# Optimization experiments

Measured on AMD Instinct MI355X. Metric: run time of the kernel, lower is better.

## Reference

```python
import jax, jax.numpy as jnp
import numpy as np

D_MODEL = 1024
H = 16
D_K = D_MODEL // H


def setup_inputs() -> dict:
    key = jax.random.key(0)
    ks = jax.random.split(key, 8)
    B, S = 2, 2048
    q = jax.random.normal(ks[0], (B, S, D_MODEL), dtype=jnp.float32)
    k = jax.random.normal(ks[1], (B, S, D_MODEL), dtype=jnp.float32)
    v = jax.random.normal(ks[2], (B, S, D_MODEL), dtype=jnp.float32)
    mask = jnp.ones((B, 1, S), dtype=jnp.int32)  # key-padding mask, 1 = keep
    sc = 1.0 / np.sqrt(D_MODEL)
    # torch Linear weights [out, in]
    Wq = jax.random.normal(ks[3], (D_MODEL, D_MODEL), dtype=jnp.float32) * sc
    Wk = jax.random.normal(ks[4], (D_MODEL, D_MODEL), dtype=jnp.float32) * sc
    Wv = jax.random.normal(ks[5], (D_MODEL, D_MODEL), dtype=jnp.float32) * sc
    Wo = jax.random.normal(ks[6], (D_MODEL, D_MODEL), dtype=jnp.float32) * sc
    return {"q": q, "k": k, "v": v, "mask": mask,
            "Wq": Wq, "Wk": Wk, "Wv": Wv, "Wo": Wo}


def reference(q, k, v, mask, Wq, Wk, Wv, Wo):
    B, Sq, _ = q.shape
    Sk = k.shape[1]
    # projections (torch Linear: x @ W.T), split heads -> [B, H, S, d_k]
    def split_heads(x, W, S):
        return (x @ W.T).reshape(B, S, H, D_K).transpose(0, 2, 1, 3)
    qh = split_heads(q, Wq, Sq)
    kh = split_heads(k, Wk, Sk)
    vh = split_heads(v, Wv, Sk)
    scores = jnp.einsum('bhqd,bhkd->bhqk', qh, kh) / jnp.sqrt(
        jnp.asarray(D_K, qh.dtype))
    # mask.unsqueeze(1): [B,1,S] -> [B,1,1,S]; masked_fill(mask==0, -1e9)
    m = mask[:, None, :, :]
    scores = jnp.where(m == 0, jnp.asarray(-1e9, scores.dtype), scores)
    p = jax.nn.softmax(scores, axis=-1)
    out = jnp.einsum('bhqk,bhkd->bhqd', p, vh)
    out = out.transpose(0, 2, 1, 3).reshape(B, Sq, H * D_K)
    return out @ Wo.T
```

## Files before the change

### kernel.cpp

```cpp
#include <hip/hip_runtime.h>
#include <hip/hip_bf16.h>

#define LOG2E 1.4426950408889634f

typedef __attribute__((ext_vector_type(8))) __bf16 bf16x8;
typedef __attribute__((ext_vector_type(2))) __bf16 bf16x2;
typedef __attribute__((ext_vector_type(4))) float f32x4;
typedef __attribute__((ext_vector_type(16))) float f32x16;

#define MFMA16(a,b,c) __builtin_amdgcn_mfma_f32_16x16x32_bf16((a),(b),(c),0,0,0)
#define MFMA32(a,b,c) __builtin_amdgcn_mfma_f32_32x32x16_bf16((a),(b),(c),0,0,0)

#define GLL16(g, l) __builtin_amdgcn_global_load_lds( \
    (const __attribute__((address_space(1))) void*)(g), \
    (__attribute__((address_space(3))) void*)(l), 16, 0, 0)

__device__ __forceinline__ unsigned short bfu(float f) {
    __bf16 h = (__bf16)f; unsigned short u; __builtin_memcpy(&u, &h, 2); return u;
}
__device__ __forceinline__ unsigned cvtpk(float lo, float hi) {
    bf16x2 t; t.x = (__bf16)lo; t.y = (__bf16)hi;
    unsigned r; __builtin_memcpy(&r, &t, 4); return r;
}
__device__ __forceinline__ bf16x8 pack4(unsigned a, unsigned b, unsigned c, unsigned d) {
    union { unsigned u[4]; bf16x8 v; } t; t.u[0]=a; t.u[1]=b; t.u[2]=c; t.u[3]=d; return t.v;
}
__device__ __forceinline__ bf16x8 cvt8(float4 a, float4 b, float s) {
    bf16x8 o;
    o[0]=(__bf16)(a.x*s); o[1]=(__bf16)(a.y*s); o[2]=(__bf16)(a.z*s); o[3]=(__bf16)(a.w*s);
    o[4]=(__bf16)(b.x*s); o[5]=(__bf16)(b.y*s); o[6]=(__bf16)(b.z*s); o[7]=(__bf16)(b.w*s);
    return o;
}

__device__ __forceinline__ size_t kidx(int bh, int s, int d) {
    int kt = s>>6, half=(s>>5)&1, l31k=s&31;
    int dc=d>>4, hik=(d>>3)&1, e=d&7;
    return (((size_t)bh*32+kt)*8 + half*4+dc)*512 + (hik*32+l31k)*8 + e;
}
__device__ __forceinline__ size_t vidx(int bh, int s, int d) {
    int kt=s>>6, kvin=s&63, kc=kvin>>4, rem=kvin&15;
    int hiv=(rem>>2)&1, e=(rem&3)+4*(rem>>3);
    int v1=d>>5, l31v=d&31;
    return (((size_t)bh*32+kt)*8 + kc*2+v1)*512 + (hiv*32+l31v)*8 + e;
}

__global__ __launch_bounds__(256)
void conv_kernel(const float* __restrict__ q, const float* __restrict__ k,
                 const float* __restrict__ v, const float* __restrict__ Wq,
                 const float* __restrict__ Wk, const float* __restrict__ Wv,
                 const float* __restrict__ Wo, unsigned short* __restrict__ Xb,
                 unsigned short* __restrict__ Wb)
{
    const int y = blockIdx.y;
    if (y < 3) {
        const float* s = (y==0)?q:(y==1)?k:v;
        size_t i = ((size_t)blockIdx.x*256 + threadIdx.x)*8;
        float4 a = *(const float4*)(s+i), b = *(const float4*)(s+i+4);
        *(bf16x8*)(Xb + (size_t)y*4194304 + i) = cvt8(a, b, 1.0f);
    } else {
        const int w = blockIdx.x >> 9;
        const float* s = (w==0)?Wq:(w==1)?Wk:(w==2)?Wv:Wo;
        const float sc = (w==0) ? 0.125f*LOG2E : 1.0f;
        size_t i = ((size_t)(blockIdx.x & 511)*256 + threadIdx.x)*8;
        float4 a = *(const float4*)(s+i), b = *(const float4*)(s+i+4);
        *(bf16x8*)(Wb + (size_t)w*1048576 + i) = cvt8(a, b, sc);
    }
}

__global__ __launch_bounds__(256)
void qkv_kernel(const unsigned short* __restrict__ Xb,
                const unsigned short* __restrict__ Wb,
                unsigned short* __restrict__ Qh, unsigned short* __restrict__ Kg,
                unsigned short* __restrict__ Vg)
{
    __shared__ unsigned short As[2][4096];
    __shared__ unsigned short Bs[2][4096];
    const int z = blockIdx.z;
    const unsigned short* X = Xb + (size_t)z*4194304;
    const unsigned short* W = Wb + (size_t)z*1048576;
    const int t = threadIdx.x, wid = t>>6, lane = t&63;
    const int m0 = blockIdx.x*128, n0 = blockIdx.y*128;
    const int wr = (wid>>1)*64, wc = (wid&1)*64;
    const int lr = lane&15, lk = lane>>4;

    f32x4 acc[4][4] = {};

#pragma unroll
    for (int i=0;i<2;++i){
        int flat = i*4096 + wid*1024 + lane*16;
        int row = flat>>6, cb = (flat&63) ^ ((row&3)<<4);
        GLL16(X + (size_t)(m0+row)*1024 + (cb>>1), (char*)&As[0][0] + i*4096 + wid*1024);
        GLL16(W + (size_t)(n0+row)*1024 + (cb>>1), (char*)&Bs[0][0] + i*4096 + wid*1024);
    }
    asm volatile("s_waitcnt vmcnt(0)" ::: "memory");
    __builtin_amdgcn_s_barrier();
    asm volatile("" ::: "memory");

    for (int kt=0; kt<32; ++kt){
        const int cur = kt&1;
        if (kt<31){
            const int nb = cur^1, K0 = (kt+1)*32;
#pragma unroll
            for (int i=0;i<2;++i){
                int flat = i*4096 + wid*1024 + lane*16;
                int row = flat>>6, cb = (flat&63) ^ ((row&3)<<4);
                GLL16(X + (size_t)(m0+row)*1024 + K0 + (cb>>1), (char*)&As[nb][0] + i*4096 + wid*1024);
                GLL16(W + (size_t)(n0+row)*1024 + K0 + (cb>>1), (char*)&Bs[nb][0] + i*4096 + wid*1024);
            }
        }
        bf16x8 a[4], b[4];
#pragma unroll
        for (int i=0;i<4;++i){
            int row = wr+i*16+lr;
            a[i] = *(const bf16x8*)((const char*)&As[cur][0] + row*64 + ((lk*16)^((row&3)<<4)));
        }
#pragma unroll
        for (int j=0;j<4;++j){
            int row = wc+j*16+lr;
            b[j] = *(const bf16x8*)((const char*)&Bs[cur][0] + row*64 + ((lk*16)^((row&3)<<4)));
        }
#pragma unroll
        for (int i=0;i<4;++i)
#pragma unroll
            for (int j=0;j<4;++j)
                acc[i][j] = MFMA16(a[i], b[j], acc[i][j]);
        asm volatile("s_waitcnt vmcnt(0)" ::: "memory");
        __builtin_amdgcn_s_barrier();
        asm volatile("" ::: "memory");
    }

#pragma unroll
    for (int i=0;i<4;++i)
#pragma unroll
      for (int j=0;j<4;++j)
#pragma unroll
        for (int r=0;r<4;++r){
            int m = m0 + wr + i*16 + lk*4 + r;
            int n = n0 + wc + j*16 + lr;
            int b_ = m>>11, s = m&2047;
            int h = n>>6, d = n&63;
            int bh = b_*16 + h;
            unsigned short val = bfu(acc[i][j][r]);
            if (z==0)      Qh[((size_t)bh*2048 + s)*64 + d] = val;
            else if (z==1) Kg[kidx(bh, s, d)] = val;
            else           Vg[vidx(bh, s, d)] = val;
        }
}

__global__ __launch_bounds__(256)
void oproj_kernel(const unsigned short* __restrict__ Oh,
                  const unsigned short* __restrict__ Wo,
                  float* __restrict__ out)
{
    __shared__ unsigned short As[2][8192];
    __shared__ unsigned short Bs2[2][4096];
    const int t = threadIdx.x, wid = t>>6, lane = t&63;
    const int m0 = blockIdx.x*128, n0 = blockIdx.y*64;
    const int wr = (wid>>1)*64, wc = (wid&1)*32;
    const int lr = lane&15, lk = lane>>4;
    const int fbase = wid*1024 + lane*16;

    f32x4 acc[4][2] = {};

#pragma unroll
    for (int i=0;i<4;++i){
        int flat = i*4096 + fbase, row = flat>>7;
        int cb = (flat&127) ^ ((row&7)<<4);
        int m = m0+row, b_ = m>>11, s = m&2047;
        GLL16(Oh + ((size_t)(b_*16+0)*2048 + s)*64 + (cb>>1), (char*)&As[0][0] + i*4096 + wid*1024);
    }
#pragma unroll
    for (int i=0;i<2;++i){
        int flat = i*4096 + fbase, row = flat>>7;
        int cb = (flat&127) ^ ((row&7)<<4);
        GLL16(Wo + (size_t)(n0+row)*1024 + (cb>>1), (char*)&Bs2[0][0] + i*4096 + wid*1024);
    }

    for (int kt=0; kt<16; ++kt){
        const int cur = kt&1;
        if (kt<15){
            const int nb = cur^1, K0 = (kt+1)*64, h = K0>>6;
#pragma unroll
            for (int i=0;i<4;++i){
                int flat = i*4096 + fbase, row = flat>>7;
                int cb = (flat&127) ^ ((row&7)<<4);
                int m = m0+row, b_ = m>>11, s = m&2047;
                GLL16(Oh + ((size_t)(b_*16+h)*2048 + s)*64 + (cb>>1),
                      (char*)&As[nb][0] + i*4096 + wid*1024);
            }
#pragma unroll
            for (int i=0;i<2;++i){
                int flat = i*4096 + fbase, row = flat>>7;
                int cb = (flat&127) ^ ((row&7)<<4);
                GLL16(Wo + (size_t)(n0+row)*1024 + K0 + (cb>>1),
                      (char*)&Bs2[nb][0] + i*4096 + wid*1024);
            }
            asm volatile("s_waitcnt vmcnt(6)" ::: "memory");
        } else {
            asm volatile("s_waitcnt vmcnt(0)" ::: "memory");
        }
        __builtin_amdgcn_s_barrier();
        asm volatile("" ::: "memory");

        bf16x8 a[4][2], b[2][2];
#pragma unroll
        for (int i=0;i<4;++i){
            int row = wr+i*16+lr, sw = (row&7)<<4;
            const char* rp = (const char*)&As[cur][0] + row*128;
#pragma unroll
            for (int ks=0;ks<2;++ks)
                a[i][ks] = *(const bf16x8*)(rp + ((ks*64 + lk*16)^sw));
        }
#pragma unroll
        for (int j=0;j<2;++j){
            int row = wc+j*16+lr, sw = (row&7)<<4;
            const char* rp = (const char*)&Bs2[cur][0] + row*128;
#pragma unroll
            for (int ks=0;ks<2;++ks)
                b[j][ks] = *(const bf16x8*)(rp + ((ks*64 + lk*16)^sw));
        }
#pragma unroll
        for (int i=0;i<4;++i)
#pragma unroll
          for (int j=0;j<2;++j)
#pragma unroll
            for (int ks=0;ks<2;++ks)
                acc[i][j] = MFMA16(a[i][ks], b[j][ks], acc[i][j]);
        asm volatile("" ::: "memory");
        __builtin_amdgcn_s_barrier();
    }

#pragma unroll
    for (int i=0;i<4;++i)
#pragma unroll
      for (int j=0;j<2;++j)
#pragma unroll
        for (int r=0;r<4;++r){
            int m = m0 + wr + i*16 + lk*4 + r;
            int n = n0 + wc + j*16 + lr;
            out[(size_t)m*1024 + n] = acc[i][j][r];
        }
}

__global__ __launch_bounds__(256, 2)
void attn_kernel(const unsigned short* __restrict__ Qh,
                 const unsigned short* __restrict__ Kg,
                 const unsigned short* __restrict__ Vg,
                 const int* __restrict__ mask,
                 unsigned short* __restrict__ Oh)
{
    const int t = threadIdx.x, wid = t >> 6, lane = t & 63;
    const int l31 = lane & 31, hi = lane >> 5;
    const int linb = blockIdx.x + 16*blockIdx.y;
    const int work = (linb & 7)*64 + (linb >> 3);
    const int bh = work >> 4;
    const int q0 = (work & 15) * 128;
    const int b_ = bh >> 4;
    const int qw = q0 + wid*32 + l31;

    unsigned flagbits;
    {
        const int4* mp = (const int4*)(mask + b_*2048 + (lane&31)*64);
        int bad = 0;
#pragma unroll
        for (int i=0;i<16;++i){ int4 m4 = mp[i];
            bad |= (m4.x==0)|(m4.y==0)|(m4.z==0)|(m4.w==0); }
        unsigned long long bm = __ballot(bad);
        flagbits = (unsigned)bm;
    }

    bf16x8 qf[4];
    const unsigned short* Qp = Qh + ((size_t)bh*2048 + qw)*64 + hi*8;
#pragma unroll
    for (int dc = 0; dc < 4; ++dc) qf[dc] = *(const bf16x8*)(Qp + dc*16);

    const unsigned short* Kb2 = Kg + (size_t)bh*131072 + lane*8;
    const unsigned short* Vb2 = Vg + (size_t)bh*131072 + lane*8;

    f32x16 o0 = {}, o1 = {}, lacc = {};
    f32x16 minit;
#pragma unroll
    for (int r = 0; r < 16; ++r) minit[r] = -12.0f;

    bf16x8 ones;
    { union { unsigned u[4]; bf16x8 v; } tt;
      tt.u[0]=tt.u[1]=tt.u[2]=tt.u[3]=0x3F803F80u; ones = tt.v; }

    auto KLOAD = [&](bf16x8* kb, int kt) {
        const unsigned short* p = Kb2 + (size_t)kt*4096;
#pragma unroll
        for (int f = 0; f < 8; ++f) kb[f] = *(const bf16x8*)(p + f*512);
    };
    auto TILE = [&](const bf16x8* kb, int kt) {
        bf16x8 vf[8];
        const unsigned short* vp = Vb2 + (size_t)kt*4096;
#pragma unroll
        for (int g = 0; g < 8; ++g) vf[g] = *(const bf16x8*)(vp + g*512);

        f32x16 s0, s1;
#pragma unroll
        for (int dc = 0; dc < 4; ++dc) {
            if (dc == 0) { s0 = MFMA32(kb[0], qf[0], minit); s1 = MFMA32(kb[4], qf[0], minit); }
            else         { s0 = MFMA32(kb[dc], qf[dc], s0);  s1 = MFMA32(kb[4+dc], qf[dc], s1); }
        }
        if (flagbits & (1u << kt)) {
            const int* mrow = mask + b_*2048 + kt*64;
#pragma unroll
            for (int r = 0; r < 16; ++r) {
                int kv = (r&3) + 8*(r>>2) + 4*hi;
                if (mrow[kv] == 0)      s0[r] = -1e9f;
                if (mrow[32 + kv] == 0) s1[r] = -1e9f;
            }
        }
#pragma unroll
        for (int r = 0; r < 16; ++r) {
            s0[r] = __builtin_amdgcn_exp2f(s0[r]);
            s1[r] = __builtin_amdgcn_exp2f(s1[r]);
        }
        bf16x8 pa[4];
        pa[0] = pack4(cvtpk(s0[0],s0[1]),  cvtpk(s0[2],s0[3]),
                      cvtpk(s0[4],s0[5]),  cvtpk(s0[6],s0[7]));
        pa[1] = pack4(cvtpk(s0[8],s0[9]),  cvtpk(s0[10],s0[11]),
                      cvtpk(s0[12],s0[13]),cvtpk(s0[14],s0[15]));
        pa[2] = pack4(cvtpk(s1[0],s1[1]),  cvtpk(s1[2],s1[3]),
                      cvtpk(s1[4],s1[5]),  cvtpk(s1[6],s1[7]));
        pa[3] = pack4(cvtpk(s1[8],s1[9]),  cvtpk(s1[10],s1[11]),
                      cvtpk(s1[12],s1[13]),cvtpk(s1[14],s1[15]));
#pragma unroll
        for (int kc = 0; kc < 4; ++kc) {
            o0   = MFMA32(pa[kc], vf[kc*2],   o0);
            o1   = MFMA32(pa[kc], vf[kc*2+1], o1);
            lacc = MFMA32(pa[kc], ones,       lacc);
        }
    };

    bf16x8 bufA[8], bufB[8];
    KLOAD(bufA, 0);
    for (int kt = 0; kt < 32; kt += 2) {
        KLOAD(bufB, kt+1);
        TILE(bufA, kt);
        if (kt+2 < 32) KLOAD(bufA, kt+2);
        TILE(bufB, kt+1);
    }

    unsigned short* Ob = Oh + ((size_t)bh*2048 + q0 + wid*32)*64;
#pragma unroll
    for (int r = 0; r < 16; ++r) {
        int qr = (r&3) + 8*(r>>2) + 4*hi;
        float inv = 1.0f / lacc[r];
        Ob[(size_t)qr*64 + l31]      = bfu(o0[r] * inv);
        Ob[(size_t)qr*64 + 32 + l31] = bfu(o1[r] * inv);
    }
}

extern "C" void kernel_launch(void* const* d_in, const int* in_sizes, int n_in,
                              void* d_out, int out_size, void* d_ws, size_t ws_size,
                              hipStream_t stream)
{
    const float* q  = (const float*)d_in[0];
    const float* k  = (const float*)d_in[1];
    const float* v  = (const float*)d_in[2];
    const int* mask = (const int*)d_in[3];
    const float* Wq = (const float*)d_in[4];
    const float* Wk = (const float*)d_in[5];
    const float* Wv = (const float*)d_in[6];
    const float* Wo = (const float*)d_in[7];
    float* out = (float*)d_out;

    unsigned short* Xb = (unsigned short*)d_ws;
    unsigned short* Wb = Xb + (size_t)12582912;
    unsigned short* Qh = Wb + (size_t)4194304;
    unsigned short* Kg = Qh + (size_t)4194304;
    unsigned short* Vg = Kg + (size_t)4194304;
    unsigned short* Oh = Xb;

    conv_kernel<<<dim3(2048,4), 256, 0, stream>>>(q, k, v, Wq, Wk, Wv, Wo, Xb, Wb);
    qkv_kernel<<<dim3(32,8,3), 256, 0, stream>>>(Xb, Wb, Qh, Kg, Vg);
    attn_kernel<<<dim3(16,32), 256, 0, stream>>>(Qh, Kg, Vg, mask, Oh);
    oproj_kernel<<<dim3(32,16), 256, 0, stream>>>(Oh, Wb + (size_t)3145728, out);
}
```

Measured before the change: 146.4 us.

## Stage K/V tiles through double-buffered LDS with async global_load_lds

Previously each wave loaded the full K and V tiles from global memory straight into registers, so all four waves fetched the same data. Now the waves share the work: each issues direct global-to-LDS loads for part of each tile into a double-buffered shared array, prefetches the next tile, waits on vmcnt and synchronises with barriers, then reads fragments from LDS. This removes redundant global and L2 traffic and register-held prefetch buffers. In exchange it adds two barriers per tile, LDS read latency and 32KB of LDS per block, which may limit occupancy at two blocks per CU.

```diff
diff --git a/kernel.cpp b/kernel.cpp
--- a/kernel.cpp
+++ b/kernel.cpp
@@ -249,6 +249,9 @@
                  const int* __restrict__ mask,
                  unsigned short* __restrict__ Oh)
 {
+    __shared__ unsigned short Ks[2][4096];
+    __shared__ unsigned short Vs[2][4096];
+
     const int t = threadIdx.x, wid = t >> 6, lane = t & 63;
     const int l31 = lane & 31, hi = lane >> 5;
     const int linb = blockIdx.x + 16*blockIdx.y;
@@ -274,8 +277,15 @@
 #pragma unroll
     for (int dc = 0; dc < 4; ++dc) qf[dc] = *(const bf16x8*)(Qp + dc*16);
 
-    const unsigned short* Kb2 = Kg + (size_t)bh*131072 + lane*8;
-    const unsigned short* Vb2 = Vg + (size_t)bh*131072 + lane*8;
+    const unsigned short* Kbase = Kg + (size_t)bh*131072;
+    const unsigned short* Vbase = Vg + (size_t)bh*131072;
+
+#pragma unroll
+    for (int i = 0; i < 2; ++i) {
+        int g = wid*2 + i;
+        GLL16(Kbase + g*512 + lane*8, &Ks[0][g*512]);
+        GLL16(Vbase + g*512 + lane*8, &Vs[0][g*512]);
+    }
 
     f32x16 o0 = {}, o1 = {}, lacc = {};
     f32x16 minit;
@@ -286,16 +296,30 @@
     { union { unsigned u[4]; bf16x8 v; } tt;
       tt.u[0]=tt.u[1]=tt.u[2]=tt.u[3]=0x3F803F80u; ones = tt.v; }
 
-    auto KLOAD = [&](bf16x8* kb, int kt) {
-        const unsigned short* p = Kb2 + (size_t)kt*4096;
-#pragma unroll
-        for (int f = 0; f < 8; ++f) kb[f] = *(const bf16x8*)(p + f*512);
-    };
-    auto TILE = [&](const bf16x8* kb, int kt) {
-        bf16x8 vf[8];
-        const unsigned short* vp = Vb2 + (size_t)kt*4096;
-#pragma unroll
-        for (int g = 0; g < 8; ++g) vf[g] = *(const bf16x8*)(vp + g*512);
+    for (int kt = 0; kt < 32; ++kt) {
+        const int cur = kt & 1;
+        if (kt < 31) {
+            const int nb = cur ^ 1;
+            const unsigned short* Kt = Kbase + (size_t)(kt+1)*4096;
+            const unsigned short* Vt2 = Vbase + (size_t)(kt+1)*4096;
+#pragma unroll
+            for (int i = 0; i < 2; ++i) {
+                int g = wid*2 + i;
+                GLL16(Kt + g*512 + lane*8, &Ks[nb][g*512]);
+                GLL16(Vt2 + g*512 + lane*8, &Vs[nb][g*512]);
+            }
+            asm volatile("s_waitcnt vmcnt(4)" ::: "memory");
+        } else {
+            asm volatile("s_waitcnt vmcnt(0)" ::: "memory");
+        }
+        __builtin_amdgcn_s_barrier();
+        asm volatile("" ::: "memory");
+
+        bf16x8 kb[8], vf[8];
+#pragma unroll
+        for (int f = 0; f < 8; ++f) kb[f] = *(const bf16x8*)&Ks[cur][f*512 + lane*8];
+#pragma unroll
+        for (int g = 0; g < 8; ++g) vf[g] = *(const bf16x8*)&Vs[cur][g*512 + lane*8];
 
         f32x16 s0, s1;
 #pragma unroll
@@ -303,6 +327,7 @@
             if (dc == 0) { s0 = MFMA32(kb[0], qf[0], minit); s1 = MFMA32(kb[4], qf[0], minit); }
             else         { s0 = MFMA32(kb[dc], qf[dc], s0);  s1 = MFMA32(kb[4+dc], qf[dc], s1); }
         }
+
         if (flagbits & (1u << kt)) {
             const int* mrow = mask + b_*2048 + kt*64;
 #pragma unroll
@@ -312,11 +337,13 @@
                 if (mrow[32 + kv] == 0) s1[r] = -1e9f;
             }
         }
+
 #pragma unroll
         for (int r = 0; r < 16; ++r) {
             s0[r] = __builtin_amdgcn_exp2f(s0[r]);
             s1[r] = __builtin_amdgcn_exp2f(s1[r]);
         }
+
         bf16x8 pa[4];
         pa[0] = pack4(cvtpk(s0[0],s0[1]),  cvtpk(s0[2],s0[3]),
                       cvtpk(s0[4],s0[5]),  cvtpk(s0[6],s0[7]));
@@ -326,21 +353,15 @@
                       cvtpk(s1[4],s1[5]),  cvtpk(s1[6],s1[7]));
         pa[3] = pack4(cvtpk(s1[8],s1[9]),  cvtpk(s1[10],s1[11]),
                       cvtpk(s1[12],s1[13]),cvtpk(s1[14],s1[15]));
+
 #pragma unroll
         for (int kc = 0; kc < 4; ++kc) {
             o0   = MFMA32(pa[kc], vf[kc*2],   o0);
             o1   = MFMA32(pa[kc], vf[kc*2+1], o1);
             lacc = MFMA32(pa[kc], ones,       lacc);
         }
-    };
-
-    bf16x8 bufA[8], bufB[8];
-    KLOAD(bufA, 0);
-    for (int kt = 0; kt < 32; kt += 2) {
-        KLOAD(bufB, kt+1);
-        TILE(bufA, kt);
-        if (kt+2 < 32) KLOAD(bufA, kt+2);
-        TILE(bufB, kt+1);
+        asm volatile("" ::: "memory");
+        __builtin_amdgcn_s_barrier();
     }
 
     unsigned short* Ob = Oh + ((size_t)bh*2048 + q0 + wid*32)*64;
```

Result: faster. 121.0 us (-17.3%).
